# Kernel tuning notes

Measured on AMD Instinct MI355X. Metric: run time of the kernel, lower is better.

## Reference

```python
import jax, jax.numpy as jnp
import numpy as np

B, T, D = 4, 4000, 1024
H = 8
DK = D // H          # key dim per head; value dim per head also DK (value_factor=1)
CHUNK = 500
EPS_LN = 1e-5
EPS_RMS = 1e-6


def rotate_every_two(x):
    x1 = x[..., ::2]
    x2 = x[..., 1::2]
    return jnp.stack((-x2, x1), axis=-1).reshape(x.shape)


def theta_shift(x, sin, cos):
    # x: [b,h,t,dk]; sin/cos: [t,dk]
    return x * cos + rotate_every_two(x) * sin


def rel_pos(slen, chunk_len, num_heads, key_dim):
    # RetNetRelPos(chunkwise_recurrent=True)
    angle = 1.0 / (10000 ** jnp.linspace(0.0, 1.0, key_dim // 2))
    angle = jnp.repeat(angle, 2)  # == unsqueeze(-1).repeat(1,2).flatten()
    decay = jnp.log(1.0 - 2.0 ** (-5.0 - jnp.arange(num_heads, dtype=jnp.float32)))
    index = jnp.arange(slen, dtype=jnp.float32)
    sin = jnp.sin(index[:, None] * angle[None, :])  # [t,dk]
    cos = jnp.cos(index[:, None] * angle[None, :])
    bi = jnp.arange(chunk_len, dtype=jnp.float32)
    tril = jnp.tril(jnp.ones((chunk_len, chunk_len), bool))
    diff = bi[:, None] - bi[None, :]
    mask = jnp.where(tril[None], jnp.exp(decay[:, None, None] * diff[None]), 0.0)  # [H,C,C]
    last_row = mask[:, -1]                                            # [H,C]
    value_inner_decay = (last_row / last_row.sum(-1, keepdims=True))[:, :, None]  # [H,C,1]
    scale = jnp.sqrt(mask.sum(-1, keepdims=True))                     # [H,C,1]
    inner_mask = mask / scale
    cross_decay = jnp.exp(decay * chunk_len)[:, None, None]           # [H,1,1]
    qid = jnp.exp(decay[:, None] * (bi + 1.0))[:, :, None]            # [H,C,1]
    query_inner_decay = qid / (scale / last_row.sum(-1)[:, None, None])
    return (sin, cos), (inner_mask, cross_decay, query_inner_decay, value_inner_decay)


def retention_chunkwise(qr, kr, v, inner):
    mask, cross_decay, query_inner_decay, value_inner_decay = inner
    b, t = v.shape[0], v.shape[1]
    C = mask.shape[1]
    n = t // C
    h, dk = qr.shape[1], qr.shape[3]
    dv = v.shape[2] // h
    # [b,h,t,dk] -> [b,n,h,C,dk]
    qr = qr.transpose(0, 2, 1, 3).reshape(b, n, C, h, dk).transpose(0, 1, 3, 2, 4)
    kr = kr.transpose(0, 2, 1, 3).reshape(b, n, C, h, dk).transpose(0, 1, 3, 2, 4)
    v = v.reshape(b, n, C, h, dv).transpose(0, 1, 3, 2, 4)  # [b,n,h,C,dv]

    qk = jnp.einsum('bnhcd,bnhed->bnhce', qr, kr) * mask  # [b,n,h,C,C]
    inner_scale = jnp.clip(jnp.abs(jax.lax.stop_gradient(qk)).sum(-1, keepdims=True), 1.0, None)
    qk = qk / inner_scale
    inner_output = jnp.einsum('bnhce,bnhed->bnhcd', qk, v)  # [b,n,h,C,dv]

    kv = jnp.einsum('bnhck,bnhcv->bnhkv', kr, v * value_inner_decay)  # [b,n,h,dk,dv]

    def step(carry, kv_i):
        kv_state, kv_scale = carry
        out = (kv_state / kv_scale, kv_scale)
        new_state = kv_state * cross_decay + kv_i
        sg = jnp.abs(jax.lax.stop_gradient(new_state)).sum(-2, keepdims=True).max(-1, keepdims=True)
        return (new_state, jnp.clip(sg, 1.0, None)), out

    init = (jnp.zeros((b, h, dk, dv), v.dtype), jnp.ones((b, h, 1, 1), v.dtype))
    _, (kv_rec, cross_scale) = jax.lax.scan(step, init, jnp.moveaxis(kv, 1, 0))
    kv_rec = jnp.moveaxis(kv_rec, 0, 1)            # [b,n,h,dk,dv]
    cross_scale = jnp.moveaxis(cross_scale, 0, 1)  # [b,n,h,1,1]

    all_scale = jnp.maximum(inner_scale, cross_scale)
    cross_output = jnp.einsum('bnhcd,bnhdv->bnhcv', qr * query_inner_decay, kv_rec)
    output = inner_output / (all_scale / inner_scale) + cross_output / (all_scale / cross_scale)
    return output.transpose(0, 1, 3, 2, 4).reshape(b, t, h, dv)  # [b,t,h,dv]


def setup_inputs() -> dict:
    key = jax.random.key(0)
    ks = jax.random.split(key, 6)
    s = 0.02
    return {
        'inputs': jax.random.normal(ks[0], (B, T, D), jnp.float32),
        'ln_gamma': jnp.ones((D,), jnp.float32),
        'ln_beta': jnp.zeros((D,), jnp.float32),
        'Wq': jax.random.normal(ks[1], (D, D), jnp.float32) * s,
        'Wk': jax.random.normal(ks[2], (D, D), jnp.float32) * s,
        'Wv': jax.random.normal(ks[3], (D, D), jnp.float32) * s,
        'Wg': jax.random.normal(ks[4], (D, D), jnp.float32) * s,
        'Wo': jax.random.normal(ks[5], (D, D), jnp.float32) * s,
    }


def reference(inputs, ln_gamma, ln_beta, Wq, Wk, Wv, Wg, Wo):
    b, t, d = inputs.shape
    # pre-LayerNorm
    mu = inputs.mean(-1, keepdims=True)
    var = ((inputs - mu) ** 2).mean(-1, keepdims=True)
    x = (inputs - mu) / jnp.sqrt(var + EPS_LN) * ln_gamma + ln_beta

    (sin, cos), inner = rel_pos(t, CHUNK, H, DK)

    q = (x @ Wq).reshape(b, t, H, DK).transpose(0, 2, 1, 3)
    k = (x @ Wk * (DK ** -0.5)).reshape(b, t, H, DK).transpose(0, 2, 1, 3)
    v = x @ Wv
    g = x @ Wg

    qr = theta_shift(q, sin, cos)
    kr = theta_shift(k, sin, cos)

    out = retention_chunkwise(qr, kr, v, inner)  # [b,t,H,dv]
    # group norm: per-head RMSNorm without affine
    out = out * jax.lax.rsqrt(jnp.mean(out ** 2, -1, keepdims=True) + EPS_RMS)
    out = out.reshape(b, t, H * DK)
    out = jax.nn.silu(g) * out
    return out @ Wo  # dropout is identity in eval
```

## Files before the change

kernel.cpp:

```cpp
#include <hip/hip_runtime.h>
#include <hip/hip_bf16.h>


typedef __attribute__((ext_vector_type(4))) float f32x4;
typedef __attribute__((ext_vector_type(8))) short s16x8;

#define DEV static __device__ __forceinline__

DEV float bfu(ushort u){ union{uint i; float f;} x; x.i=((uint)u)<<16; return x.f; }
DEV float bflo(uint w){ union{uint i; float f;} x; x.i=w<<16; return x.f; }
DEV float bfhi(uint w){ union{uint i; float f;} x; x.i=w&0xffff0000u; return x.f; }
DEV ushort f2bf(float f){ union{float f; uint u;} x; x.f=f; uint r = x.u + 0x7fffu + ((x.u>>16)&1u); return (ushort)(r>>16); }
DEV uint pack2(float lo, float hi){ return ((uint)f2bf(hi)<<16) | (uint)f2bf(lo); }
DEV void unpack8(uint4 u, float* f){
  f[0]=bflo(u.x); f[1]=bfhi(u.x); f[2]=bflo(u.y); f[3]=bfhi(u.y);
  f[4]=bflo(u.z); f[5]=bfhi(u.z); f[6]=bflo(u.w); f[7]=bfhi(u.w);
}
DEV void cstore(float* C, size_t i, float v){ C[i]=v; }
DEV void cstore(ushort* C, size_t i, float v){ C[i]=f2bf(v); }

DEV void gload16(const ushort* g, ushort* l) {
  __builtin_amdgcn_global_load_lds((const __attribute__((address_space(1))) void*)g,
                                   (__attribute__((address_space(3))) void*)l, 16, 0, 0);
}

__global__ __launch_bounds__(256) void f2bf_t_kernel(const float* __restrict__ src,
                                                     ushort* __restrict__ dst) {
  __shared__ ushort t[64][72];
  int kt = blockIdx.x*64, nt = blockIdx.y*64;
  int tid = threadIdx.x;
  int r = tid>>2, c0 = (tid&3)*16;
  const float* s = src + (size_t)(kt+r)*1024 + nt + c0;
  #pragma unroll
  for (int j=0;j<16;j+=4) {
    float4 vv = *(const float4*)(s+j);
    t[r][c0+j]=f2bf(vv.x); t[r][c0+j+1]=f2bf(vv.y); t[r][c0+j+2]=f2bf(vv.z); t[r][c0+j+3]=f2bf(vv.w);
  }
  __syncthreads();
  union { uint4 u4[2]; ushort s16[16]; } tmp;
  #pragma unroll
  for (int j=0;j<16;j++) tmp.s16[j] = t[c0+j][r];
  ushort* d = dst + (size_t)(nt+r)*1024 + kt + c0;
  *(uint4*)(d)   = tmp.u4[0];
  *(uint4*)(d+8) = tmp.u4[1];
}

__global__ __launch_bounds__(256) void ln_kernel(const float* __restrict__ x,
                                                 const float* __restrict__ gamma,
                                                 const float* __restrict__ beta,
                                                 ushort* __restrict__ xo) {
  int row = blockIdx.x;
  int tid = threadIdx.x;
  const float* xr = x + (size_t)row*1024;
  float4 u = ((const float4*)xr)[tid];
  float s = u.x+u.y+u.z+u.w;
  float sq = u.x*u.x+u.y*u.y+u.z*u.z+u.w*u.w;
  #pragma unroll
  for (int o=32;o;o>>=1){ s += __shfl_xor(s,o); sq += __shfl_xor(sq,o); }
  __shared__ float red[8];
  int wv=tid>>6, ln=tid&63;
  if (ln==0){ red[wv]=s; red[4+wv]=sq; }
  __syncthreads();
  s = red[0]+red[1]+red[2]+red[3];
  sq = red[4]+red[5]+red[6]+red[7];
  float mu = s*(1.0f/1024.0f);
  float var = sq*(1.0f/1024.0f)-mu*mu;
  float inv = rsqrtf(var+1e-5f);
  float4 gg = ((const float4*)gamma)[tid];
  float4 bb = ((const float4*)beta)[tid];
  float o0=(u.x-mu)*inv*gg.x+bb.x;
  float o1=(u.y-mu)*inv*gg.y+bb.y;
  float o2=(u.z-mu)*inv*gg.z+bb.z;
  float o3=(u.w-mu)*inv*gg.w+bb.w;
  uint2 w; w.x=pack2(o0,o1); w.y=pack2(o2,o3);
  ((uint2*)(xo+(size_t)row*1024))[tid]=w;
}

__global__ __launch_bounds__(256) void sincos_kernel(float* __restrict__ sint, float* __restrict__ cost) {
  int idx = blockIdx.x*256+threadIdx.x;
  if (idx >= 4000*64) return;
  int t = idx>>6, i = idx&63;
  float ang = expf(-9.210340371976184f * (float)i * (1.0f/63.0f));
  float a = (float)t * ang;
  float sv = sinf(a), cv = cosf(a);
  sint[(size_t)t*128+2*i] = sv; sint[(size_t)t*128+2*i+1] = sv;
  cost[(size_t)t*128+2*i] = cv; cost[(size_t)t*128+2*i+1] = cv;
}

template<typename OutT>
__global__ __launch_bounds__(256) void gemm_bt(const ushort* __restrict__ A,
                                               const ushort* __restrict__ BT,
                                               OutT* __restrict__ C,
                                               int M, int N, int K) {
  __shared__ ushort As[8192];
  __shared__ ushort Bs[8192];
  int ny = N>>7;
  int cpx = ((M>>7)*ny)>>3;
  int wg = blockIdx.x;
  int orig = (wg&7)*cpx + (wg>>3);
  int bm = (orig>>3)*128, bn = (orig&7)*128;
  int tid = threadIdx.x;
  int w = tid>>6, l = tid&63;
  int wm = (w>>1)*64, wn = (w&1)*64;
  int rsel = l&15, ko = (l>>4)*8;
  f32x4 acc[4][4];
  #pragma unroll
  for (int i=0;i<4;i++)
    #pragma unroll
    for (int j=0;j<4;j++){ acc[i][j][0]=0; acc[i][j][1]=0; acc[i][j][2]=0; acc[i][j][3]=0; }
  const ushort* ap0 = A  + (size_t)(bm + w*32 + (l>>2))*K + (l&3)*8;
  const ushort* ap1 = ap0 + (size_t)16*K;
  const ushort* bp0 = BT + (size_t)(bn + w*32 + (l>>2))*K + (l&3)*8;
  const ushort* bp1 = bp0 + (size_t)16*K;
  {
    ushort* ab = As + w*1024; ushort* bb = Bs + w*1024;
    gload16(ap0, ab); gload16(ap1, ab+512);
    gload16(bp0, bb); gload16(bp1, bb+512);
  }
  int cur = 0;
  for (int kt=0; kt<K; kt+=32) {
    __syncthreads();
    if (kt+32 < K) {
      int nb = cur^1;
      ushort* ab = As + nb*4096 + w*1024; ushort* bb = Bs + nb*4096 + w*1024;
      gload16(ap0+kt+32, ab); gload16(ap1+kt+32, ab+512);
      gload16(bp0+kt+32, bb); gload16(bp1+kt+32, bb+512);
    }
    const ushort* Ac = As + cur*4096;
    const ushort* Bc = Bs + cur*4096;
    s16x8 af[4], bfr[4];
    #pragma unroll
    for (int mf=0;mf<4;mf++) af[mf]  = *(const s16x8*)&Ac[(wm+mf*16+rsel)*32 + ko];
    #pragma unroll
    for (int nf=0;nf<4;nf++) bfr[nf] = *(const s16x8*)&Bc[(wn+nf*16+rsel)*32 + ko];
    #pragma unroll
    for (int mf=0;mf<4;mf++)
      #pragma unroll
      for (int nf=0;nf<4;nf++)
        acc[mf][nf] = __builtin_amdgcn_mfma_f32_16x16x32_bf16(af[mf], bfr[nf], acc[mf][nf], 0,0,0);
    cur ^= 1;
  }
  int crow = bm+wm+(l>>4)*4;
  int ccol = bn+wn+(l&15);
  #pragma unroll
  for (int mf=0;mf<4;mf++)
    #pragma unroll
    for (int nf=0;nf<4;nf++)
      #pragma unroll
      for (int r2=0;r2<4;r2++)
        cstore(C, (size_t)(crow+mf*16+r2)*N + ccol+nf*16, acc[mf][nf][r2]);
}

__global__ __launch_bounds__(256) void qrot_kernel(ushort* __restrict__ q,
                                                   const float* __restrict__ sint,
                                                   const float* __restrict__ cost) {
  int idx = blockIdx.x*256+threadIdx.x;
  if (idx >= 16000*512) return;
  int row = idx>>9, cp = idx&511;
  int col = cp*2;
  int t = row - (row/4000)*4000;
  int d = col & 127, h = col>>7;
  int r_rel = t - (t/500)*500;
  float decay = logf(1.0f - exp2f(-5.0f-(float)h));
  float qs = expf(decay*(float)r_rel);
  float c = cost[(size_t)t*128+d], s = sint[(size_t)t*128+d];
  uint* qp = (uint*)(q + (size_t)row*1024 + col);
  uint w = *qp;
  float q0=bflo(w), q1=bfhi(w);
  *qp = pack2((q0*c - q1*s)*qs, (q1*c + q0*s)*qs);
}

__global__ __launch_bounds__(256) void kvT_kernel(ushort* __restrict__ k,
                                                  const ushort* __restrict__ v,
                                                  ushort* __restrict__ kT,
                                                  ushort* __restrict__ vT,
                                                  const float* __restrict__ sint,
                                                  const float* __restrict__ cost) {
  int bnh = blockIdx.x, ct = blockIdx.y;
  int h = bnh&7, n=(bnh>>3)&7, b=bnh>>6;
  size_t base = (size_t)(b*4000+n*500)*1024 + h*128;
  float decay = logf(1.0f - exp2f(-5.0f-(float)h));
  __shared__ ushort ktl[64][136];
  __shared__ ushort vtl[64][136];
  int tid = threadIdx.x;
  int srow = tid>>2, sc0 = (tid&3)*32;
  int c = ct*64 + srow;
  if (c < 500) {
    int t = n*500 + c;
    float ksc = expf(-decay*(float)c) * 0.08838834764831845f;
    ushort* kp = k + base + (size_t)c*1024 + sc0;
    const ushort* vp = v + base + (size_t)c*1024 + sc0;
    #pragma unroll
    for (int j=0;j<4;j++) {
      uint4 kw = *(const uint4*)(kp+j*8);
      float kf[8]; unpack8(kw,kf);
      uint4 ko4;
      uint* kou = (uint*)&ko4;
      #pragma unroll
      for (int p=0;p<4;p++) {
        int d = sc0+j*8+2*p;
        float cc = cost[(size_t)t*128+d], ss = sint[(size_t)t*128+d];
        float r0 = (kf[2*p]*cc - kf[2*p+1]*ss)*ksc;
        float r1 = (kf[2*p+1]*cc + kf[2*p]*ss)*ksc;
        kou[p] = pack2(r0,r1);
      }
      *(uint4*)&ktl[srow][sc0+j*8] = ko4;
      *(uint4*)(kp+j*8) = ko4;
      *(uint4*)&vtl[srow][sc0+j*8] = *(const uint4*)(vp+j*8);
    }
  } else {
    uint4 z; z.x=0;z.y=0;z.z=0;z.w=0;
    #pragma unroll
    for (int j=0;j<4;j++){ *(uint4*)&ktl[srow][sc0+j*8]=z; *(uint4*)&vtl[srow][sc0+j*8]=z; }
  }
  __syncthreads();
  int d = tid>>1, ch = (tid&1)*32;
  union{uint4 u4[4]; ushort s[32];} pk, pv_;
  #pragma unroll
  for (int j=0;j<32;j++){ pk.s[j] = ktl[ch+j][d]; pv_.s[j] = vtl[ch+j][d]; }
  ushort* kd = kT + (size_t)bnh*65536 + (size_t)d*512 + ct*64 + ch;
  ushort* vd = vT + (size_t)bnh*65536 + (size_t)d*512 + ct*64 + ch;
  #pragma unroll
  for (int j=0;j<4;j++){ *(uint4*)(kd+j*8) = pk.u4[j]; *(uint4*)(vd+j*8) = pv_.u4[j]; }
}

__global__ __launch_bounds__(256) void kv_mfma(const ushort* __restrict__ kT,
                                               const ushort* __restrict__ vT,
                                               float* __restrict__ kvp) {
  int bnh = blockIdx.x;
  __shared__ ushort sh2[16384];
  int tid=threadIdx.x;
  int wv=tid>>6, l=tid&63, g=l>>4, c16=l&15;
  int wr = wv>>1, wc = wv&1;
  int ri[4], ro[4];
  #pragma unroll
  for (int jj=0;jj<4;jj++){
    int i = wv*256 + jj*64 + l;
    ri[jj] = i>>3;
    ro[jj] = (((i&7)*16) ^ ((ri[jj]&7)<<4))>>1;
  }
  const ushort* kbase = kT + (size_t)bnh*65536;
  const ushort* vbase = vT + (size_t)bnh*65536;
  f32x4 acc[4][4];
  #pragma unroll
  for (int i=0;i<4;i++)
    #pragma unroll
    for (int j=0;j<4;j++){ acc[i][j][0]=0; acc[i][j][1]=0; acc[i][j][2]=0; acc[i][j][3]=0; }
  for (int ctep=0; ctep<8; ctep++) {
    int cb = ctep*64;
    __syncthreads();
    #pragma unroll
    for (int jj=0;jj<4;jj++){
      gload16(kbase + (size_t)ri[jj]*512 + cb + ro[jj], (ushort*)((char*)sh2 + wv*4096 + jj*1024));
      gload16(vbase + (size_t)ri[jj]*512 + cb + ro[jj], (ushort*)((char*)sh2 + 16384 + wv*4096 + jj*1024));
    }
    __syncthreads();
    #pragma unroll
    for (int kc=0;kc<2;kc++) {
      s16x8 af[4], bf2[4];
      #pragma unroll
      for (int mf=0;mf<4;mf++){
        int row = wr*64+mf*16+c16;
        af[mf] = *(const s16x8*)((const char*)sh2 + row*128 + ((((kc*32+g*8)*2)) ^ ((row&7)<<4)));
      }
      #pragma unroll
      for (int nf=0;nf<4;nf++){
        int row = wc*64+nf*16+c16;
        bf2[nf] = *(const s16x8*)((const char*)sh2 + 16384 + row*128 + ((((kc*32+g*8)*2)) ^ ((row&7)<<4)));
      }
      #pragma unroll
      for (int mf=0;mf<4;mf++)
        #pragma unroll
        for (int nf=0;nf<4;nf++)
          acc[mf][nf] = __builtin_amdgcn_mfma_f32_16x16x32_bf16(af[mf], bf2[nf], acc[mf][nf], 0,0,0);
    }
  }
  float* outp = kvp + (size_t)bnh*16384;
  #pragma unroll
  for (int mf=0;mf<4;mf++)
    #pragma unroll
    for (int nf=0;nf<4;nf++)
      #pragma unroll
      for (int reg=0;reg<4;reg++)
        outp[(size_t)(wr*64+mf*16+g*4+reg)*128 + wc*64+nf*16+c16] = acc[mf][nf][reg];
}

__global__ __launch_bounds__(256) void scan_kernel(const float* __restrict__ kvp,
                                                   ushort* __restrict__ kvrecT,
                                                   float* __restrict__ crosssc) {
  int bh = blockIdx.x;
  int b = bh>>3, h = bh&7;
  float Dh = 1.0f - exp2f(-5.0f-(float)h);
  float decay = logf(Dh);
  float cd = expf(decay*500.0f);
  float ls = (1.0f - expf(decay*500.0f))/(1.0f-Dh);
  float cst = expf(decay*499.0f)/ls;
  int tid=threadIdx.x;
  int vcol = tid&127, khalf = tid>>7;
  float st[64];
  #pragma unroll
  for (int i=0;i<64;i++) st[i]=0;
  float scale = 1.0f;
  __shared__ float colpart[2][128];
  __shared__ float sred[2];
  for (int n=0;n<8;n++) {
    int bnh = (b*8+n)*8+h;
    const float* src = kvp + (size_t)bnh*16384;
    ushort* rec = kvrecT + (size_t)bnh*16384;
    float inv = 1.0f/scale;
    float cs = 0;
    #pragma unroll
    for (int i=0;i<64;i++) {
      int kk = khalf*64+i;
      rec[(size_t)vcol*128+kk] = f2bf(st[i]*inv);
      st[i] = st[i]*cd + cst*src[(size_t)kk*128+vcol];
      cs += fabsf(st[i]);
    }
    if (tid==0) crosssc[bnh] = scale;
    colpart[khalf][vcol] = cs;
    __syncthreads();
    if (tid<128) colpart[0][tid] += colpart[1][tid];
    __syncthreads();
    float m = (tid<128)? colpart[0][tid] : 0.0f;
    #pragma unroll
    for (int o=32;o;o>>=1) m = fmaxf(m,__shfl_xor(m,o));
    if (tid<128 && (tid&63)==0) sred[tid>>6]=m;
    __syncthreads();
    scale = fmaxf(fmaxf(sred[0],sred[1]),1.0f);
    __syncthreads();
  }
}

__global__ __launch_bounds__(256,4) void iout_mfma(const ushort* __restrict__ qr,
                                                   const ushort* __restrict__ kr,
                                                   const ushort* __restrict__ vT,
                                                   const ushort* __restrict__ kvrecT,
                                                   const float* __restrict__ crosssc,
                                                   const ushort* __restrict__ gbuf,
                                                   ushort* __restrict__ opre) {
  int bnh = blockIdx.x, rt = blockIdx.y;
  int h = bnh&7, n=(bnh>>3)&7, b=bnh>>6;
  size_t base = (size_t)(b*4000+n*500)*1024 + h*128;
  float Dh = 1.0f - exp2f(-5.0f-(float)h);
  float decay = logf(Dh);
  __shared__ ushort sh[20480];
  char* shb = (char*)sh;
  int tid = threadIdx.x;
  int wv = tid>>6, l = tid&63;
  int g = l>>4, c16 = l&15;
  int r_base = rt*64 + wv*16 + g*4;

  int qrow = rt*64 + wv*16 + c16; if (qrow>499) qrow=499;
  s16x8 aq[4];
  #pragma unroll
  for (int kc=0;kc<4;kc++)
    aq[kc] = *(const s16x8*)(qr + base + (size_t)qrow*1024 + kc*32 + g*8);

  int ktrow[4], ktofs[4], vtrow[4], vtofs[4];
  #pragma unroll
  for (int jj=0;jj<4;jj++){
    int i = wv*256 + jj*64 + l;
    int r_ = i>>4;  ktrow[jj]=r_;  ktofs[jj] = (((i&15)*16) ^ ((r_&7)<<4))>>1;
    int r2_ = i>>3; vtrow[jj]=r2_; vtofs[jj] = (((i&7)*16) ^ ((r2_&7)<<4))>>1;
  }
  const ushort* vTb = vT + (size_t)bnh*65536;

  f32x4 pv[8], cc[8];
  #pragma unroll
  for (int i=0;i<8;i++){
    #pragma unroll
    for (int j=0;j<4;j++){ pv[i][j]=0.0f; cc[i][j]=0.0f; }
  }
  float rowsum[4] = {0,0,0,0};

  for (int et=0; et<=rt; et++) {
    __syncthreads();
    #pragma unroll
    for (int jj=0;jj<4;jj++){
      int gr = et*64 + ktrow[jj]; if (gr>499) gr=499;
      gload16(kr + base + (size_t)gr*1024 + ktofs[jj], (ushort*)(shb + wv*4096 + jj*1024));
      gload16(vTb + (size_t)vtrow[jj]*512 + et*64 + vtofs[jj], (ushort*)(shb + 16384 + wv*4096 + jj*1024));
    }
    __syncthreads();
    f32x4 S[4];
    #pragma unroll
    for (int i=0;i<4;i++){ S[i][0]=0; S[i][1]=0; S[i][2]=0; S[i][3]=0; }
    #pragma unroll
    for (int kc=0;kc<4;kc++) {
      #pragma unroll
      for (int ni=0;ni<4;ni++) {
        int krow = ni*16+c16;
        s16x8 bf = *(const s16x8*)(shb + krow*256 + ((((kc*32+g*8)*2)) ^ ((krow&7)<<4)));
        S[ni] = __builtin_amdgcn_mfma_f32_16x16x32_bf16(aq[kc], bf, S[ni], 0,0,0);
      }
    }
    bool diag = (et==rt);
    #pragma unroll
    for (int ni=0;ni<4;ni++) {
      int e_rel = et*64 + ni*16 + c16;
      #pragma unroll
      for (int reg=0;reg<4;reg++) {
        float p = S[ni][reg];
        if (diag && e_rel > r_base+reg) p = 0.0f;
        rowsum[reg] += fabsf(p);
        int prow = wv*16 + g*4 + reg;
        *(ushort*)(shb + 32768 + prow*128 + (((ni*16+c16)*2) ^ ((prow&7)<<4))) = f2bf(p);
      }
    }
    #pragma unroll
    for (int kc=0;kc<2;kc++) {
      int prow = wv*16 + c16;
      s16x8 pa = *(const s16x8*)(shb + 32768 + prow*128 + ((((kc*32+g*8)*2)) ^ ((prow&7)<<4)));
      #pragma unroll
      for (int nf=0;nf<8;nf++) {
        int vrow = nf*16+c16;
        s16x8 vb = *(const s16x8*)(shb + 16384 + vrow*128 + ((((kc*32+g*8)*2)) ^ ((vrow&7)<<4)));
        pv[nf] = __builtin_amdgcn_mfma_f32_16x16x32_bf16(pa, vb, pv[nf], 0,0,0);
      }
    }
  }
  #pragma unroll
  for (int reg=0;reg<4;reg++) {
    float s = rowsum[reg];
    s += __shfl_xor(s,1); s += __shfl_xor(s,2); s += __shfl_xor(s,4); s += __shfl_xor(s,8);
    rowsum[reg] = s;
  }
  __syncthreads();
  #pragma unroll
  for (int jj=0;jj<8;jj++){
    int i = wv*512 + jj*64 + l;
    int r_ = i>>4;
    int ofs = (((i&15)*16) ^ ((r_&7)<<4))>>1;
    gload16(kvrecT + (size_t)bnh*16384 + (size_t)r_*128 + ofs, (ushort*)(shb + wv*8192 + jj*1024));
  }
  __syncthreads();
  #pragma unroll
  for (int kc=0;kc<4;kc++) {
    #pragma unroll
    for (int nf=0;nf<8;nf++) {
      int krow = nf*16+c16;
      s16x8 bb = *(const s16x8*)(shb + krow*256 + ((((kc*32+g*8)*2)) ^ ((krow&7)<<4)));
      cc[nf] = __builtin_amdgcn_mfma_f32_16x16x32_bf16(aq[kc], bb, cc[nf], 0,0,0);
    }
  }
  float cs = crosssc[bnh];
  float lsum = (1.0f-expf(decay*500.0f))/(1.0f-Dh);
  float ed = expf(decay);
  #pragma unroll
  for (int reg=0;reg<4;reg++) {
    int rr = r_base + reg;
    if (rr < 500) {
      float rs = (1.0f-expf(decay*(float)(rr+1)))/(1.0f-Dh);
      float rsr = rsqrtf(rs);
      float is = fmaxf(1.0f, rowsum[reg]*rsr);
      float all = fmaxf(is, cs);
      float qid = ed*lsum*rsr;
      float fi = rsr/all;
      float fc = qid*(cs/all);
      float o[8]; float ssq = 0.0f;
      #pragma unroll
      for (int nf=0;nf<8;nf++){ o[nf] = pv[nf][reg]*fi + cc[nf][reg]*fc; ssq += o[nf]*o[nf]; }
      ssq += __shfl_xor(ssq,1); ssq += __shfl_xor(ssq,2); ssq += __shfl_xor(ssq,4); ssq += __shfl_xor(ssq,8);
      float rmss = rsqrtf(ssq*(1.0f/128.0f)+1e-6f);
      size_t rowoff = (size_t)(b*4000+n*500+rr)*1024 + h*128;
      #pragma unroll
      for (int nf=0;nf<8;nf++){
        float gv = bfu(gbuf[rowoff + nf*16 + c16]);
        float sg = gv/(1.0f+expf(-gv));
        opre[rowoff + nf*16 + c16] = f2bf(sg*o[nf]*rmss);
      }
    }
  }
}

extern "C" void kernel_launch(void* const* d_in, const int* in_sizes, int n_in,
                              void* d_out, int out_size, void* d_ws, size_t ws_size,
                              hipStream_t stream) {
  const float* x     = (const float*)d_in[0];
  const float* gamma = (const float*)d_in[1];
  const float* beta  = (const float*)d_in[2];
  const float* Wq    = (const float*)d_in[3];
  const float* Wk    = (const float*)d_in[4];
  const float* Wv    = (const float*)d_in[5];
  const float* Wg    = (const float*)d_in[6];
  const float* Wo    = (const float*)d_in[7];
  float* out = (float*)d_out;

  char* ws = (char*)d_ws;
  size_t off = 0;
  auto alloc = [&](size_t bytes)->void* { void* p = ws+off; off += (bytes+255)&~(size_t)255; return p; };
  const size_t BT1024 = (size_t)16000*1024;
  ushort* xln  = (ushort*)alloc(BT1024*2);
  ushort* q    = (ushort*)alloc(BT1024*2);
  ushort* k    = (ushort*)alloc(BT1024*2);
  ushort* v    = (ushort*)alloc(BT1024*2);
  ushort* g    = (ushort*)alloc(BT1024*2);
  ushort* WqT  = (ushort*)alloc((size_t)1024*1024*2);
  ushort* WkT  = (ushort*)alloc((size_t)1024*1024*2);
  ushort* WvT  = (ushort*)alloc((size_t)1024*1024*2);
  ushort* WgT  = (ushort*)alloc((size_t)1024*1024*2);
  ushort* WoT  = (ushort*)alloc((size_t)1024*1024*2);
  float* sint  = (float*)alloc((size_t)4000*128*4);
  float* cost  = (float*)alloc((size_t)4000*128*4);
  ushort* kT   = (ushort*)alloc((size_t)256*65536*2);
  ushort* vT   = (ushort*)alloc((size_t)256*65536*2);
  ushort* kvrecT=(ushort*)alloc((size_t)256*16384*2);
  float* crosssc = (float*)alloc(256*4);
  (void)ws_size; (void)in_sizes; (void)n_in; (void)out_size;

  ln_kernel<<<16000,256,0,stream>>>(x,gamma,beta,xln);
  sincos_kernel<<<1000,256,0,stream>>>(sint,cost);
  dim3 tt(16,16);
  f2bf_t_kernel<<<tt,256,0,stream>>>(Wq,WqT);
  f2bf_t_kernel<<<tt,256,0,stream>>>(Wk,WkT);
  f2bf_t_kernel<<<tt,256,0,stream>>>(Wv,WvT);
  f2bf_t_kernel<<<tt,256,0,stream>>>(Wg,WgT);
  f2bf_t_kernel<<<tt,256,0,stream>>>(Wo,WoT);

  gemm_bt<ushort><<<1000,256,0,stream>>>(xln,WqT,q,16000,1024,1024);
  gemm_bt<ushort><<<1000,256,0,stream>>>(xln,WkT,k,16000,1024,1024);
  gemm_bt<ushort><<<1000,256,0,stream>>>(xln,WvT,v,16000,1024,1024);
  gemm_bt<ushort><<<1000,256,0,stream>>>(xln,WgT,g,16000,1024,1024);

  qrot_kernel<<<32000,256,0,stream>>>(q,sint,cost);
  dim3 gkt(256,8);
  kvT_kernel<<<gkt,256,0,stream>>>(k,v,kT,vT,sint,cost);

  float* kvp = (float*)xln;
  kv_mfma<<<256,256,0,stream>>>(kT,vT,kvp);
  scan_kernel<<<32,256,0,stream>>>(kvp,kvrecT,crosssc);

  ushort* opre = xln;
  dim3 gr(256,8);
  iout_mfma<<<gr,256,0,stream>>>(q,k,vT,kvrecT,crosssc,g,opre);

  gemm_bt<float><<<1000,256,0,stream>>>(opre,WoT,out,16000,1024,1024);
}
```

Measured before the change: 478.6 us.

## Fuse rotary, decay scaling and K/V transposes into projection GEMM epilogues

The q-rotation and k/v transpose kernels are removed. Rotary embedding, the decay scaling and the transposed kT/vT writes now happen inside the projection GEMM epilogues, using a lane shuffle to pair rotary elements. This drops a full read and write pass over q, k and v plus two launches, and the separate v buffer. Because the old transpose no longer zero-pads kT/vT, kv_mfma zeroes the tail columns in LDS for the last chunk. Other changes: the five weight conversions become one launch, iout blocks are remapped to a 1D grid, and s_setprio is raised around MFMA loops. The scattered 2-byte transposed stores in the epilogue may be poorly coalesced.

Result: faster. 453.2 us (-5.3%).

```diff
diff --git a/kernel.cpp b/kernel.cpp
--- a/kernel.cpp
+++ b/kernel.cpp
@@ -8,24 +8,28 @@
 #define DEV static __device__ __forceinline__
 
 DEV float bfu(ushort u){ union{uint i; float f;} x; x.i=((uint)u)<<16; return x.f; }
-DEV float bflo(uint w){ union{uint i; float f;} x; x.i=w<<16; return x.f; }
-DEV float bfhi(uint w){ union{uint i; float f;} x; x.i=w&0xffff0000u; return x.f; }
 DEV ushort f2bf(float f){ union{float f; uint u;} x; x.f=f; uint r = x.u + 0x7fffu + ((x.u>>16)&1u); return (ushort)(r>>16); }
 DEV uint pack2(float lo, float hi){ return ((uint)f2bf(hi)<<16) | (uint)f2bf(lo); }
-DEV void unpack8(uint4 u, float* f){
-  f[0]=bflo(u.x); f[1]=bfhi(u.x); f[2]=bflo(u.y); f[3]=bfhi(u.y);
-  f[4]=bflo(u.z); f[5]=bfhi(u.z); f[6]=bflo(u.w); f[7]=bfhi(u.w);
-}
-DEV void cstore(float* C, size_t i, float v){ C[i]=v; }
-DEV void cstore(ushort* C, size_t i, float v){ C[i]=f2bf(v); }
 
 DEV void gload16(const ushort* g, ushort* l) {
   __builtin_amdgcn_global_load_lds((const __attribute__((address_space(1))) void*)g,
                                    (__attribute__((address_space(3))) void*)l, 16, 0, 0);
 }
 
-__global__ __launch_bounds__(256) void f2bf_t_kernel(const float* __restrict__ src,
-                                                     ushort* __restrict__ dst) {
+__global__ __launch_bounds__(256) void f2bf_t_all(const float* __restrict__ s0, const float* __restrict__ s1,
+                                                  const float* __restrict__ s2, const float* __restrict__ s3,
+                                                  const float* __restrict__ s4,
+                                                  ushort* __restrict__ d0, ushort* __restrict__ d1,
+                                                  ushort* __restrict__ d2, ushort* __restrict__ d3,
+                                                  ushort* __restrict__ d4) {
+  const float* src; ushort* dst;
+  switch (blockIdx.z) {
+    case 0: src=s0; dst=d0; break;
+    case 1: src=s1; dst=d1; break;
+    case 2: src=s2; dst=d2; break;
+    case 3: src=s3; dst=d3; break;
+    default: src=s4; dst=d4; break;
+  }
   __shared__ ushort t[64][72];
   int kt = blockIdx.x*64, nt = blockIdx.y*64;
   int tid = threadIdx.x;
@@ -87,10 +91,13 @@
   cost[(size_t)t*128+2*i] = cv; cost[(size_t)t*128+2*i+1] = cv;
 }
 
-template<typename OutT>
+template<int EPI>
 __global__ __launch_bounds__(256) void gemm_bt(const ushort* __restrict__ A,
                                                const ushort* __restrict__ BT,
-                                               OutT* __restrict__ C,
+                                               void* __restrict__ Cv,
+                                               ushort* __restrict__ kTout,
+                                               const float* __restrict__ sint,
+                                               const float* __restrict__ cost,
                                                int M, int N, int K) {
   __shared__ ushort As[8192];
   __shared__ ushort Bs[8192];
@@ -140,88 +147,61 @@
         acc[mf][nf] = __builtin_amdgcn_mfma_f32_16x16x32_bf16(af[mf], bfr[nf], acc[mf][nf], 0,0,0);
     cur ^= 1;
   }
-  int crow = bm+wm+(l>>4)*4;
-  int ccol = bn+wn+(l&15);
-  #pragma unroll
-  for (int mf=0;mf<4;mf++)
-    #pragma unroll
-    for (int nf=0;nf<4;nf++)
-      #pragma unroll
-      for (int r2=0;r2<4;r2++)
-        cstore(C, (size_t)(crow+mf*16+r2)*N + ccol+nf*16, acc[mf][nf][r2]);
-}
-
-__global__ __launch_bounds__(256) void qrot_kernel(ushort* __restrict__ q,
-                                                   const float* __restrict__ sint,
-                                                   const float* __restrict__ cost) {
-  int idx = blockIdx.x*256+threadIdx.x;
-  if (idx >= 16000*512) return;
-  int row = idx>>9, cp = idx&511;
-  int col = cp*2;
-  int t = row - (row/4000)*4000;
-  int d = col & 127, h = col>>7;
-  int r_rel = t - (t/500)*500;
-  float decay = logf(1.0f - exp2f(-5.0f-(float)h));
-  float qs = expf(decay*(float)r_rel);
-  float c = cost[(size_t)t*128+d], s = sint[(size_t)t*128+d];
-  uint* qp = (uint*)(q + (size_t)row*1024 + col);
-  uint w = *qp;
-  float q0=bflo(w), q1=bfhi(w);
-  *qp = pack2((q0*c - q1*s)*qs, (q1*c + q0*s)*qs);
-}
-
-__global__ __launch_bounds__(256) void kvT_kernel(ushort* __restrict__ k,
-                                                  const ushort* __restrict__ v,
-                                                  ushort* __restrict__ kT,
-                                                  ushort* __restrict__ vT,
-                                                  const float* __restrict__ sint,
-                                                  const float* __restrict__ cost) {
-  int bnh = blockIdx.x, ct = blockIdx.y;
-  int h = bnh&7, n=(bnh>>3)&7, b=bnh>>6;
-  size_t base = (size_t)(b*4000+n*500)*1024 + h*128;
-  float decay = logf(1.0f - exp2f(-5.0f-(float)h));
-  __shared__ ushort ktl[64][136];
-  __shared__ ushort vtl[64][136];
-  int tid = threadIdx.x;
-  int srow = tid>>2, sc0 = (tid&3)*32;
-  int c = ct*64 + srow;
-  if (c < 500) {
-    int t = n*500 + c;
-    float ksc = expf(-decay*(float)c) * 0.08838834764831845f;
-    ushort* kp = k + base + (size_t)c*1024 + sc0;
-    const ushort* vp = v + base + (size_t)c*1024 + sc0;
-    #pragma unroll
-    for (int j=0;j<4;j++) {
-      uint4 kw = *(const uint4*)(kp+j*8);
-      float kf[8]; unpack8(kw,kf);
-      uint4 ko4;
-      uint* kou = (uint*)&ko4;
-      #pragma unroll
-      for (int p=0;p<4;p++) {
-        int d = sc0+j*8+2*p;
-        float cc = cost[(size_t)t*128+d], ss = sint[(size_t)t*128+d];
-        float r0 = (kf[2*p]*cc - kf[2*p+1]*ss)*ksc;
-        float r1 = (kf[2*p+1]*cc + kf[2*p]*ss)*ksc;
-        kou[p] = pack2(r0,r1);
-      }
-      *(uint4*)&ktl[srow][sc0+j*8] = ko4;
-      *(uint4*)(kp+j*8) = ko4;
-      *(uint4*)&vtl[srow][sc0+j*8] = *(const uint4*)(vp+j*8);
-    }
-  } else {
-    uint4 z; z.x=0;z.y=0;z.z=0;z.w=0;
-    #pragma unroll
-    for (int j=0;j<4;j++){ *(uint4*)&ktl[srow][sc0+j*8]=z; *(uint4*)&vtl[srow][sc0+j*8]=z; }
-  }
-  __syncthreads();
-  int d = tid>>1, ch = (tid&1)*32;
-  union{uint4 u4[4]; ushort s[32];} pk, pv_;
-  #pragma unroll
-  for (int j=0;j<32;j++){ pk.s[j] = ktl[ch+j][d]; pv_.s[j] = vtl[ch+j][d]; }
-  ushort* kd = kT + (size_t)bnh*65536 + (size_t)d*512 + ct*64 + ch;
-  ushort* vd = vT + (size_t)bnh*65536 + (size_t)d*512 + ct*64 + ch;
-  #pragma unroll
-  for (int j=0;j<4;j++){ *(uint4*)(kd+j*8) = pk.u4[j]; *(uint4*)(vd+j*8) = pv_.u4[j]; }
+  int crow0 = bm+wm+(l>>4)*4;
+  int ccol0 = bn+wn+(l&15);
+  #pragma unroll
+  for (int mf=0;mf<4;mf++) {
+    #pragma unroll
+    for (int nf=0;nf<4;nf++) {
+      int col = ccol0 + nf*16;
+      if constexpr (EPI==0) {
+        ushort* C = (ushort*)Cv;
+        #pragma unroll
+        for (int r2=0;r2<4;r2++)
+          C[(size_t)(crow0+mf*16+r2)*N + col] = f2bf(acc[mf][nf][r2]);
+      } else if constexpr (EPI==1) {
+        float* C = (float*)Cv;
+        #pragma unroll
+        for (int r2=0;r2<4;r2++)
+          C[(size_t)(crow0+mf*16+r2)*N + col] = acc[mf][nf][r2];
+      } else if constexpr (EPI==2 || EPI==3) {
+        ushort* C = (ushort*)Cv;
+        int h = col>>7, d = col&127;
+        float decay = logf(1.0f - exp2f(-5.0f-(float)h));
+        #pragma unroll
+        for (int r2=0;r2<4;r2++) {
+          int row = crow0+mf*16+r2;
+          int t = row - (row/4000)*4000;
+          float cc = cost[(size_t)t*128+d], ss = sint[(size_t)t*128+d];
+          float vv = acc[mf][nf][r2];
+          float ov = __shfl_xor(vv, 1);
+          float rot = ((l&1)==0) ? (vv*cc - ov*ss) : (vv*cc + ov*ss);
+          int cch = t - (t/500)*500;
+          if constexpr (EPI==2) {
+            rot *= expf(decay*(float)cch);
+            C[(size_t)row*N + col] = f2bf(rot);
+          } else {
+            rot *= expf(-decay*(float)cch) * 0.08838834764831845f;
+            ushort rb = f2bf(rot);
+            C[(size_t)row*N + col] = rb;
+            int bnh = (row/4000)*64 + (t/500)*8 + h;
+            kTout[(size_t)bnh*65536 + (size_t)d*512 + cch] = rb;
+          }
+        }
+      } else {
+        ushort* vTo = (ushort*)Cv;
+        int h = col>>7, d = col&127;
+        #pragma unroll
+        for (int r2=0;r2<4;r2++) {
+          int row = crow0+mf*16+r2;
+          int t = row - (row/4000)*4000;
+          int bnh = (row/4000)*64 + (t/500)*8 + h;
+          int cch = t - (t/500)*500;
+          vTo[(size_t)bnh*65536 + (size_t)d*512 + cch] = f2bf(acc[mf][nf][r2]);
+        }
+      }
+    }
+  }
 }
 
 __global__ __launch_bounds__(256) void kv_mfma(const ushort* __restrict__ kT,
@@ -255,6 +235,13 @@
       gload16(vbase + (size_t)ri[jj]*512 + cb + ro[jj], (ushort*)((char*)sh2 + 16384 + wv*4096 + jj*1024));
     }
     __syncthreads();
+    if (ctep==7) {
+      for (int z=tid; z<128*12; z+=256) {
+        int r = z/12, j = 52 + (z - (z/12)*12);
+        *(ushort*)((char*)sh2 + 16384 + r*128 + ((j*2) ^ ((r&7)<<4))) = 0;
+      }
+      __syncthreads();
+    }
     #pragma unroll
     for (int kc=0;kc<2;kc++) {
       s16x8 af[4], bf2[4];
@@ -338,7 +325,10 @@
                                                    const float* __restrict__ crosssc,
                                                    const ushort* __restrict__ gbuf,
                                                    ushort* __restrict__ opre) {
-  int bnh = blockIdx.x, rt = blockIdx.y;
+  int ib = blockIdx.x;
+  int x = ib&7, u = ib>>3;
+  int rt = u&7;
+  int bnh = x*32 + (u>>3);
   int h = bnh&7, n=(bnh>>3)&7, b=bnh>>6;
   size_t base = (size_t)(b*4000+n*500)*1024 + h*128;
   float Dh = 1.0f - exp2f(-5.0f-(float)h);
@@ -385,6 +375,7 @@
     f32x4 S[4];
     #pragma unroll
     for (int i=0;i<4;i++){ S[i][0]=0; S[i][1]=0; S[i][2]=0; S[i][3]=0; }
+    __builtin_amdgcn_s_setprio(1);
     #pragma unroll
     for (int kc=0;kc<4;kc++) {
       #pragma unroll
@@ -394,6 +385,7 @@
         S[ni] = __builtin_amdgcn_mfma_f32_16x16x32_bf16(aq[kc], bf, S[ni], 0,0,0);
       }
     }
+    __builtin_amdgcn_s_setprio(0);
     bool diag = (et==rt);
     #pragma unroll
     for (int ni=0;ni<4;ni++) {
@@ -407,6 +399,7 @@
         *(ushort*)(shb + 32768 + prow*128 + (((ni*16+c16)*2) ^ ((prow&7)<<4))) = f2bf(p);
       }
     }
+    __builtin_amdgcn_s_setprio(1);
     #pragma unroll
     for (int kc=0;kc<2;kc++) {
       int prow = wv*16 + c16;
@@ -418,6 +411,7 @@
         pv[nf] = __builtin_amdgcn_mfma_f32_16x16x32_bf16(pa, vb, pv[nf], 0,0,0);
       }
     }
+    __builtin_amdgcn_s_setprio(0);
   }
   #pragma unroll
   for (int reg=0;reg<4;reg++) {
@@ -434,6 +428,7 @@
     gload16(kvrecT + (size_t)bnh*16384 + (size_t)r_*128 + ofs, (ushort*)(shb + wv*8192 + jj*1024));
   }
   __syncthreads();
+  __builtin_amdgcn_s_setprio(1);
   #pragma unroll
   for (int kc=0;kc<4;kc++) {
     #pragma unroll
@@ -443,6 +438,7 @@
       cc[nf] = __builtin_amdgcn_mfma_f32_16x16x32_bf16(aq[kc], bb, cc[nf], 0,0,0);
     }
   }
+  __builtin_amdgcn_s_setprio(0);
   float cs = crosssc[bnh];
   float lsum = (1.0f-expf(decay*500.0f))/(1.0f-Dh);
   float ed = expf(decay);
@@ -493,7 +489,6 @@
   ushort* xln  = (ushort*)alloc(BT1024*2);
   ushort* q    = (ushort*)alloc(BT1024*2);
   ushort* k    = (ushort*)alloc(BT1024*2);
-  ushort* v    = (ushort*)alloc(BT1024*2);
   ushort* g    = (ushort*)alloc(BT1024*2);
   ushort* WqT  = (ushort*)alloc((size_t)1024*1024*2);
   ushort* WkT  = (ushort*)alloc((size_t)1024*1024*2);
@@ -510,29 +505,20 @@
 
   ln_kernel<<<16000,256,0,stream>>>(x,gamma,beta,xln);
   sincos_kernel<<<1000,256,0,stream>>>(sint,cost);
-  dim3 tt(16,16);
-  f2bf_t_kernel<<<tt,256,0,stream>>>(Wq,WqT);
-  f2bf_t_kernel<<<tt,256,0,stream>>>(Wk,WkT);
-  f2bf_t_kernel<<<tt,256,0,stream>>>(Wv,WvT);
-  f2bf_t_kernel<<<tt,256,0,stream>>>(Wg,WgT);
-  f2bf_t_kernel<<<tt,256,0,stream>>>(Wo,WoT);
-
-  gemm_bt<ushort><<<1000,256,0,stream>>>(xln,WqT,q,16000,1024,1024);
-  gemm_bt<ushort><<<1000,256,0,stream>>>(xln,WkT,k,16000,1024,1024);
-  gemm_bt<ushort><<<1000,256,0,stream>>>(xln,WvT,v,16000,1024,1024);
-  gemm_bt<ushort><<<1000,256,0,stream>>>(xln,WgT,g,16000,1024,1024);
-
-  qrot_kernel<<<32000,256,0,stream>>>(q,sint,cost);
-  dim3 gkt(256,8);
-  kvT_kernel<<<gkt,256,0,stream>>>(k,v,kT,vT,sint,cost);
+  dim3 tt(16,16,5);
+  f2bf_t_all<<<tt,256,0,stream>>>(Wq,Wk,Wv,Wg,Wo, WqT,WkT,WvT,WgT,WoT);
+
+  gemm_bt<2><<<1000,256,0,stream>>>(xln,WqT,(void*)q, nullptr,sint,cost,16000,1024,1024);
+  gemm_bt<3><<<1000,256,0,stream>>>(xln,WkT,(void*)k, kT,     sint,cost,16000,1024,1024);
+  gemm_bt<4><<<1000,256,0,stream>>>(xln,WvT,(void*)vT,nullptr,sint,cost,16000,1024,1024);
+  gemm_bt<0><<<1000,256,0,stream>>>(xln,WgT,(void*)g, nullptr,sint,cost,16000,1024,1024);
 
   float* kvp = (float*)xln;
   kv_mfma<<<256,256,0,stream>>>(kT,vT,kvp);
   scan_kernel<<<32,256,0,stream>>>(kvp,kvrecT,crosssc);
 
   ushort* opre = xln;
-  dim3 gr(256,8);
-  iout_mfma<<<gr,256,0,stream>>>(q,k,vT,kvrecT,crosssc,g,opre);
-
-  gemm_bt<float><<<1000,256,0,stream>>>(opre,WoT,out,16000,1024,1024);
-}
+  iout_mfma<<<2048,256,0,stream>>>(q,k,vT,kvrecT,crosssc,g,opre);
+
+  gemm_bt<1><<<1000,256,0,stream>>>(opre,WoT,(void*)out,nullptr,sint,cost,16000,1024,1024);
+}
```
